# Optimization experiments

Hardware: AMD Instinct MI355X
Metric: run time of the kernel (lower is better)

The kernel has to match this reference:

```python
import jax, jax.numpy as jnp
import numpy as np

B, N, A = 8, 16384, 7
NUM_GROUP = 1024   # npoint / G
GROUP_SIZE = 32    # knn k / M


def setup_inputs() -> dict:
    key = jax.random.key(0)
    xyz = jax.random.uniform(key, (B, N, A), dtype=jnp.float32)
    return {"xyz": xyz}


def _farthest_point_sample(xyz, npoint):
    # xyz: [B, N, A]; distances computed on first 3 dims only.
    b, n, a = xyz.shape
    coords = xyz[:, :, :3]
    batch = jnp.arange(b)
    # Deterministic start index (original uses randint; any start is a valid FPS seed).
    init = (jnp.full((b, n), 1e10, dtype=xyz.dtype), jnp.zeros((b,), dtype=jnp.int32))

    def step(carry, _):
        distance, farthest = carry
        centroid = xyz[batch, farthest]                      # [B, A]
        d = jnp.sum((coords - centroid[:, None, :3]) ** 2, -1)  # [B, N]
        distance = jnp.minimum(distance, d)                  # masked update == min
        new_farthest = jnp.argmax(distance, axis=-1).astype(jnp.int32)
        return (distance, new_farthest), (farthest, centroid)

    _, (idxs, cents) = jax.lax.scan(step, init, None, length=npoint)
    centroids = jnp.swapaxes(idxs, 0, 1)        # [B, npoint]
    centroids_attrs = jnp.swapaxes(cents, 0, 1)  # [B, npoint, A]
    return centroids, centroids_attrs


def _knn(center, xyz, k):
    # Euclidean cdist over ALL A attributes (as in the original torch.cdist call).
    # Squared distance preserves topk ordering.
    c2 = jnp.sum(center ** 2, -1)[:, :, None]    # [B, G, 1]
    x2 = jnp.sum(xyz ** 2, -1)[:, None, :]       # [B, 1, N]
    d2 = c2 + x2 - 2.0 * jnp.einsum('bga,bna->bgn', center, xyz)  # [B, G, N]
    _, idx = jax.lax.top_k(-d2, k)               # smallest-k, ascending distance
    return idx


def reference(xyz):
    center_idx, centroids_attrs = _farthest_point_sample(xyz, NUM_GROUP)
    centroids_coors = centroids_attrs[:, :, :3]
    idx = _knn(centroids_attrs, xyz, GROUP_SIZE)             # [B, G, M]
    b = xyz.shape[0]
    neighborhood = xyz[jnp.arange(b)[:, None, None], idx]    # [B, G, M, A]
    neighborhood = jnp.concatenate(
        [neighborhood[..., :3] - centroids_coors[:, :, None, :],
         neighborhood[..., 3:]], axis=-1)
    return neighborhood, center_idx, centroids_attrs, centroids_coors
```

## Files before the change

### kernel.cpp

```cpp
#include <hip/hip_runtime.h>

#define N_PTS  16384
#define B_SZ   8
#define NGROUP 1024
#define KNN_K  32
#define ATTR   7

#define OFF_NB     0
#define OFF_IDX    (B_SZ * NGROUP * KNN_K * ATTR)
#define OFF_CATTR  (OFF_IDX + B_SZ * NGROUP)
#define OFF_CCOORD (OFF_CATTR + B_SZ * NGROUP * ATTR)

typedef float v2f __attribute__((ext_vector_type(2)));
typedef float v4f __attribute__((ext_vector_type(4)));
typedef float f2u __attribute__((ext_vector_type(2), aligned(4)));

template <int CTRL>
__device__ __forceinline__ float fmax_dpp_step(float x) {
    int d = __builtin_amdgcn_update_dpp(__float_as_int(x), __float_as_int(x),
                                        CTRL, 0xf, 0xf, false);
    return fmaxf(x, __int_as_float(d));
}
template <int CTRL>
__device__ __forceinline__ unsigned umin_dpp_step(unsigned x) {
    unsigned d = (unsigned)__builtin_amdgcn_update_dpp((int)x, (int)x,
                                                       CTRL, 0xf, 0xf, false);
    return x < d ? x : d;
}

__device__ __forceinline__ float wave_max_f32(float x) {
    x = fmax_dpp_step<0x111>(x);
    x = fmax_dpp_step<0x112>(x);
    x = fmax_dpp_step<0x114>(x);
    x = fmax_dpp_step<0x118>(x);
    x = fmax_dpp_step<0x142>(x);
    x = fmax_dpp_step<0x143>(x);
    return __int_as_float(__builtin_amdgcn_readlane(__float_as_int(x), 63));
}
__device__ __forceinline__ unsigned wave_min_u32(unsigned x) {
    x = umin_dpp_step<0x111>(x);
    x = umin_dpp_step<0x112>(x);
    x = umin_dpp_step<0x114>(x);
    x = umin_dpp_step<0x118>(x);
    x = umin_dpp_step<0x142>(x);
    x = umin_dpp_step<0x143>(x);
    return (unsigned)__builtin_amdgcn_readlane((int)x, 63);
}

__global__ void prep_kernel(const float* __restrict__ xyz, float* __restrict__ x2,
                            float* __restrict__ xt) {
#pragma clang fp contract(off)
    int i = blockIdx.x * blockDim.x + threadIdx.x;
    if (i >= B_SZ * N_PTS) return;
    const int b = i >> 14;
    const int p = i & (N_PTS - 1);
    const float* q = xyz + (size_t)i * ATTR;
    f2u a01 = *(const f2u*)q;
    f2u a23 = *(const f2u*)(q + 2);
    f2u a45 = *(const f2u*)(q + 4);
    float a6 = q[6];
    float s = a01.x * a01.x;
    s = s + a01.y * a01.y;
    s = s + a23.x * a23.x;
    s = s + a23.y * a23.y;
    s = s + a45.x * a45.x;
    s = s + a45.y * a45.y;
    s = s + a6 * a6;
    x2[i] = s;
    float* T = xt + (size_t)b * ATTR * N_PTS + p;
    T[0 * N_PTS] = a01.x;
    T[1 * N_PTS] = a01.y;
    T[2 * N_PTS] = a23.x;
    T[3 * N_PTS] = a23.y;
    T[4 * N_PTS] = a45.x;
    T[5 * N_PTS] = a45.y;
    T[6 * N_PTS] = a6;
}

#define FOR8(M) M(0) M(1) M(2) M(3) M(4) M(5) M(6) M(7)

#define PT_DECL(J) v2f pz##J, pd##J; v4f ra##J, rb##J;

#define STAGE(J) { \
    const int q = t + (J << 10); \
    const float* r0 = X + (size_t)(q << 1) * ATTR; \
    f2u u0 = *(const f2u*)r0;          float z0 = r0[2]; \
    f2u u1 = *(const f2u*)(r0 + ATTR); float z1 = r0[2 + ATTR]; \
    const v4f xy4 = (v4f){u0.x, u1.x, u0.y, u1.y}; \
    lxy[q] = xy4; \
    ra##J = xy4; \
    rb##J = xy4; \
    pz##J = (v2f){z0, z1}; \
    pd##J = (v2f){1e10f, 1e10f}; }

#define SCAN1(J, RC, RN) { \
    RN##J = lxy[t + (J << 10)]; \
    const v4f xy = RC##J; \
    v2f dx = (v2f){xy.x, xy.y} - cx2; \
    v2f dy = (v2f){xy.z, xy.w} - cy2; \
    v2f dz = pz##J - cz2; \
    v2f a  = dx * dx; \
    a = a + dy * dy; \
    a = a + dz * dz; \
    v2f nd; \
    nd.x = fminf(pd##J.x, a.x); \
    nd.y = fminf(pd##J.y, a.y); \
    pd##J = nd; \
    if (nd.x > best) { best = nd.x; bidx = (t << 1) + (J << 11); } \
    if (nd.y > best) { best = nd.y; bidx = (t << 1) + (J << 11) + 1; } }

#define FPS_SCAN(RC, RN) \
    SCAN1(0, RC, RN) SCAN1(1, RC, RN) SCAN1(2, RC, RN) SCAN1(3, RC, RN) \
    SCAN1(4, RC, RN) SCAN1(5, RC, RN) SCAN1(6, RC, RN) SCAN1(7, RC, RN)

#define FPS_STEP(SVAL, RC, RN) { \
    const int s_ = (SVAL); \
    const v2f cx2 = {cx, cx}, cy2 = {cy, cy}, cz2 = {cz, cz}; \
    float best = -1.0f; \
    int   bidx = 0; \
    FPS_SCAN(RC, RN) \
    const float wm = wave_max_f32(best); \
    const unsigned cand = (best == wm) ? (unsigned)bidx : 0xFFFFFFFFu; \
    const unsigned widx = wave_min_u32(cand); \
    if (lane == 0) { \
        const unsigned long long key = \
            ((unsigned long long)__float_as_uint(wm) << 32) | \
            (unsigned)(N_PTS - widx); \
        atomicMax(&slot[s_ % 3], key); \
    } \
    if (t == 0) slot[(s_ + 1) % 3] = 0ull; \
    __syncthreads(); \
    const unsigned long long bk = slot[s_ % 3]; \
    const int win = N_PTS - (int)(unsigned)bk; \
    const int sbidx = __builtin_amdgcn_readfirstlane(win); \
    if (t == 0) sel[s_ + 1] = sbidx; \
    const float* qw = X + (size_t)sbidx * ATTR; \
    cx = qw[0]; cy = qw[1]; cz = qw[2]; }

__global__ __launch_bounds__(1024)
void fps_kernel(const float* __restrict__ xyz, float* __restrict__ out) {
#pragma clang fp contract(off)
    const int b = blockIdx.x;
    const int t = threadIdx.x;
    const int lane = t & 63;
    const float* X = xyz + (size_t)b * N_PTS * ATTR;

    __shared__ v4f lxy[N_PTS / 2];
    __shared__ int sel[NGROUP];
    __shared__ unsigned long long slot[3];

    FOR8(PT_DECL)
    FOR8(STAGE)

    if (t == 0) { slot[0] = 0ull; sel[0] = 0; }
    float cx = X[0], cy = X[1], cz = X[2];
    __syncthreads();

    for (int s = 0; s < NGROUP - 2; s += 2) {
        FPS_STEP(s,     ra, rb)
        FPS_STEP(s + 1, rb, ra)
    }
    FPS_STEP(NGROUP - 2, ra, rb)
    __syncthreads();

    {
        const int g = t;
        const int idx = sel[g];
        const float* q = X + (size_t)idx * ATTR;
        float a0 = q[0], a1 = q[1], a2 = q[2], a3 = q[3], a4 = q[4], a5 = q[5], a6 = q[6];
        out[OFF_IDX + b * NGROUP + g] = (float)idx;
        float* ca = out + OFF_CATTR + (size_t)(b * NGROUP + g) * ATTR;
        ca[0] = a0; ca[1] = a1; ca[2] = a2; ca[3] = a3; ca[4] = a4; ca[5] = a5; ca[6] = a6;
        float* cc = out + OFF_CCOORD + (size_t)(b * NGROUP + g) * 3;
        cc[0] = a0; cc[1] = a1; cc[2] = a2;
    }
}

__device__ __forceinline__ void topk_insert(float d2, int p, int lane,
                                            float& ld, int& li, float& kd, int& ki) {
    const bool cand = (d2 < kd) || (d2 == kd && p < ki);
    unsigned long long mask = __ballot(cand);
    while (mask) {
        const int l = __ffsll(mask) - 1;
        mask &= mask - 1;
        const float dc = __shfl(d2, l);
        const int   pc = __shfl(p, l);
        if ((dc < kd) || (dc == kd && pc < ki)) {
            const bool before = (ld < dc) || (ld == dc && li < pc);
            const int pos = (int)__popcll(__ballot(before));
            const float sd = __shfl_up(ld, 1);
            const int   si = __shfl_up(li, 1);
            if (lane == pos)      { ld = dc; li = pc; }
            else if (lane > pos)  { ld = sd; li = si; }
            if (lane >= KNN_K)    { ld = __builtin_inff(); li = 0x7fffffff; }
            kd = __shfl(ld, KNN_K - 1);
            ki = __shfl(li, KNN_K - 1);
        }
    }
}

__global__ __launch_bounds__(256) void knn_kernel(const float* __restrict__ xyz,
                                                  const float* __restrict__ x2,
                                                  const float* __restrict__ xt,
                                                  float* __restrict__ out) {
#pragma clang fp contract(off)
    const int lane = threadIdx.x & 63;
    const int gg = blockIdx.x * 4 + (threadIdx.x >> 6);
    const int b  = gg >> 10;
    const float* X = xyz + (size_t)b * N_PTS * ATTR;

    const float* C = out + OFF_CATTR + (size_t)gg * ATTR;
    const float c0 = C[0], c1 = C[1], c2a = C[2], c3 = C[3], c4 = C[4], c5 = C[5], c6 = C[6];
    float csq = c0 * c0;
    csq = csq + c1 * c1;
    csq = csq + c2a * c2a;
    csq = csq + c3 * c3;
    csq = csq + c4 * c4;
    csq = csq + c5 * c5;
    csq = csq + c6 * c6;

    float ld = __builtin_inff();
    int   li = 0x7fffffff;
    float kd = __builtin_inff();
    int   ki = 0x7fffffff;

    if (xt != nullptr) {
        const float* T0 = xt + (size_t)b * ATTR * N_PTS;
        const float* T1 = T0 + N_PTS;
        const float* T2 = T1 + N_PTS;
        const float* T3 = T2 + N_PTS;
        const float* T4 = T3 + N_PTS;
        const float* T5 = T4 + N_PTS;
        const float* T6 = T5 + N_PTS;
        const float* XB = x2 + (size_t)b * N_PTS;
        for (int p0 = 0; p0 < N_PTS; p0 += 64) {
            const int p = p0 + lane;
            const float q0 = T0[p], q1 = T1[p], q2 = T2[p], q3 = T3[p];
            const float q4 = T4[p], q5 = T5[p], q6 = T6[p];
            float dot = c0 * q0;
            dot = dot + c1 * q1;
            dot = dot + c2a * q2;
            dot = dot + c3 * q3;
            dot = dot + c4 * q4;
            dot = dot + c5 * q5;
            dot = dot + c6 * q6;
            const float xx = XB[p];
            const float d2 = (csq + xx) - 2.0f * dot;
            topk_insert(d2, p, lane, ld, li, kd, ki);
        }
    } else {
        for (int p0 = 0; p0 < N_PTS; p0 += 64) {
            const int p = p0 + lane;
            const float* q = X + (size_t)p * ATTR;
            float dot = c0 * q[0];
            dot = dot + c1 * q[1];
            dot = dot + c2a * q[2];
            dot = dot + c3 * q[3];
            dot = dot + c4 * q[4];
            dot = dot + c5 * q[5];
            dot = dot + c6 * q[6];
            float xx = q[0] * q[0];
            xx = xx + q[1] * q[1];
            xx = xx + q[2] * q[2];
            xx = xx + q[3] * q[3];
            xx = xx + q[4] * q[4];
            xx = xx + q[5] * q[5];
            xx = xx + q[6] * q[6];
            const float d2 = (csq + xx) - 2.0f * dot;
            topk_insert(d2, p, lane, ld, li, kd, ki);
        }
    }

    if (lane < KNN_K) {
        const float* q = X + (size_t)li * ATTR;
        float* o = out + OFF_NB + ((size_t)gg * KNN_K + lane) * ATTR;
        o[0] = q[0] - c0;
        o[1] = q[1] - c1;
        o[2] = q[2] - c2a;
        o[3] = q[3];
        o[4] = q[4];
        o[5] = q[5];
        o[6] = q[6];
    }
}

extern "C" void kernel_launch(void* const* d_in, const int* in_sizes, int n_in,
                              void* d_out, int out_size, void* d_ws, size_t ws_size,
                              hipStream_t stream) {
    const float* xyz = (const float*)d_in[0];
    float* out = (float*)d_out;

    const size_t need = (size_t)(B_SZ * N_PTS) * (1 + ATTR) * sizeof(float);
    const bool use_ws = ws_size >= need;
    float* x2 = use_ws ? (float*)d_ws : nullptr;
    float* xt = use_ws ? ((float*)d_ws + B_SZ * N_PTS) : nullptr;

    if (use_ws) {
        prep_kernel<<<(B_SZ * N_PTS + 255) / 256, 256, 0, stream>>>(xyz, x2, xt);
    }
    fps_kernel<<<B_SZ, 1024, 0, stream>>>(xyz, out);
    knn_kernel<<<(B_SZ * NGROUP) / 4, 256, 0, stream>>>(xyz, x2, xt, out);
}
```

Before: 1.988 ms.

## Replace shared atomicMax FPS reduction with per-wave slots and DPP cross-wave max

Each wave now writes its best key and the winning point's coordinates into a double-buffered shared slot array instead of doing an atomicMax on a shared 64-bit slot. After the barrier, every wave reduces the 16 keys with a DPP row reduction to find the winner. It then reads the centroid coordinates from shared memory rather than global memory. A ballot fast path skips the index min-reduction when there is no tie. This removes the atomic, the slot reset and a dependent global load from the serial per-step critical path, at the cost of extra register selects and a 16-entry DPP reduction in every wave.

```diff
diff --git a/kernel.cpp b/kernel.cpp
--- a/kernel.cpp
+++ b/kernel.cpp
@@ -45,6 +45,19 @@
     x = umin_dpp_step<0x142>(x);
     x = umin_dpp_step<0x143>(x);
     return (unsigned)__builtin_amdgcn_readlane((int)x, 63);
+}
+
+template <int CTRL>
+__device__ __forceinline__ void kmax_dpp_step(unsigned long long& k, int& r) {
+    int lo = __builtin_amdgcn_update_dpp((int)(unsigned)k, (int)(unsigned)k,
+                                         CTRL, 0xf, 0xf, false);
+    int hi = __builtin_amdgcn_update_dpp((int)(unsigned)(k >> 32),
+                                         (int)(unsigned)(k >> 32),
+                                         CTRL, 0xf, 0xf, false);
+    int rr = __builtin_amdgcn_update_dpp(r, r, CTRL, 0xf, 0xf, false);
+    const unsigned long long kk =
+        ((unsigned long long)(unsigned)hi << 32) | (unsigned)lo;
+    if (kk > k) { k = kk; r = rr; }
 }
 
 __global__ void prep_kernel(const float* __restrict__ xyz, float* __restrict__ x2,
@@ -115,27 +128,54 @@
 
 #define FPS_STEP(SVAL, RC, RN) { \
     const int s_ = (SVAL); \
+    const int par = s_ & 1; \
     const v2f cx2 = {cx, cx}, cy2 = {cy, cy}, cz2 = {cz, cz}; \
     float best = -1.0f; \
     int   bidx = 0; \
     FPS_SCAN(RC, RN) \
+     \
+    const int Jw = (bidx >> 11) & 7; \
+    const v4f xyw = lxy[t + (Jw << 10)]; \
+    v2f t01 = (Jw & 1) ? pz1 : pz0; \
+    v2f t23 = (Jw & 1) ? pz3 : pz2; \
+    v2f t45 = (Jw & 1) ? pz5 : pz4; \
+    v2f t67 = (Jw & 1) ? pz7 : pz6; \
+    v2f u0s = (Jw & 2) ? t23 : t01; \
+    v2f u1s = (Jw & 2) ? t67 : t45; \
+    v2f vzs = (Jw & 4) ? u1s : u0s; \
+    const float zw = (bidx & 1) ? vzs.y : vzs.x; \
+     \
     const float wm = wave_max_f32(best); \
-    const unsigned cand = (best == wm) ? (unsigned)bidx : 0xFFFFFFFFu; \
-    const unsigned widx = wave_min_u32(cand); \
-    if (lane == 0) { \
-        const unsigned long long key = \
-            ((unsigned long long)__float_as_uint(wm) << 32) | \
-            (unsigned)(N_PTS - widx); \
-        atomicMax(&slot[s_ % 3], key); \
+    const unsigned long long mtie = __ballot(best == wm); \
+    int wl; \
+    if (__popcll(mtie) == 1) { \
+        wl = (int)__ffsll((unsigned long long)mtie) - 1; \
+    } else { \
+        const unsigned cand = (best == wm) ? (unsigned)bidx : 0xFFFFFFFFu; \
+        const unsigned widx = wave_min_u32(cand); \
+        wl = (int)__ffsll(__ballot(cand == widx)) - 1; \
     } \
-    if (t == 0) slot[(s_ + 1) % 3] = 0ull; \
+    if (lane == wl) { \
+         \
+        kbuf[par][w] = ((unsigned long long)__float_as_uint(best) << 32) | \
+                       (unsigned)(N_PTS - bidx); \
+        const float xw = (bidx & 1) ? xyw.y : xyw.x; \
+        const float yw = (bidx & 1) ? xyw.w : xyw.z; \
+        cbuf[par][w] = (v4f){xw, yw, zw, 0.0f}; \
+    } \
     __syncthreads(); \
-    const unsigned long long bk = slot[s_ % 3]; \
-    const int win = N_PTS - (int)(unsigned)bk; \
-    const int sbidx = __builtin_amdgcn_readfirstlane(win); \
-    if (t == 0) sel[s_ + 1] = sbidx; \
-    const float* qw = X + (size_t)sbidx * ATTR; \
-    cx = qw[0]; cy = qw[1]; cz = qw[2]; }
+     \
+    unsigned long long bk = kbuf[par][lane & 15]; \
+    int rr = lane & 15; \
+    kmax_dpp_step<0x111>(bk, rr); \
+    kmax_dpp_step<0x112>(bk, rr); \
+    kmax_dpp_step<0x114>(bk, rr); \
+    kmax_dpp_step<0x118>(bk, rr); \
+    const int rwin = __builtin_amdgcn_readlane(rr, 15); \
+    const int klo  = __builtin_amdgcn_readlane((int)(unsigned)bk, 15); \
+    if (t == 0) sel[s_ + 1] = N_PTS - (int)(unsigned)klo; \
+    const v4f wc = cbuf[par][rwin]; \
+    cx = wc.x; cy = wc.y; cz = wc.z; }
 
 __global__ __launch_bounds__(1024)
 void fps_kernel(const float* __restrict__ xyz, float* __restrict__ out) {
@@ -143,16 +183,18 @@
     const int b = blockIdx.x;
     const int t = threadIdx.x;
     const int lane = t & 63;
+    const int w = t >> 6;
     const float* X = xyz + (size_t)b * N_PTS * ATTR;
 
     __shared__ v4f lxy[N_PTS / 2];
     __shared__ int sel[NGROUP];
-    __shared__ unsigned long long slot[3];
+    __shared__ unsigned long long kbuf[2][16];
+    __shared__ v4f cbuf[2][16];
 
     FOR8(PT_DECL)
     FOR8(STAGE)
 
-    if (t == 0) { slot[0] = 0ull; sel[0] = 0; }
+    if (t == 0) sel[0] = 0;
     float cx = X[0], cy = X[1], cz = X[2];
     __syncthreads();
 
```

After: 2.309 ms. 1.16x slower.
